# Kernel optimization log

Hardware: AMD Instinct MI355X
Metric: run time of the kernel (lower is better)

## Reference

```python
import jax, jax.numpy as jnp
import numpy as np

S, N, K = 8, 2048, 64          # snapshots, atoms, max neighbors (sum of max_num_neighs)
L = 20.0                        # periodic box length
R_CS, R_C = 6.0, 12.0           # smooth cutoff radii
M2 = 16                         # dim_sub_net


def _mlp(x, params, resnet=False):
    # DenseChainNet: Linear -> relu per layer; resnet skip when dims match or double (DeepMD style)
    for W, b in params:
        y = jax.nn.relu(x @ W + b)
        if resnet and y.shape[-1] == x.shape[-1]:
            y = y + x
        elif resnet and y.shape[-1] == 2 * x.shape[-1]:
            y = y + jnp.concatenate([x, x], axis=-1)
        x = y
    return x


def setup_inputs() -> dict:
    ks = jax.random.split(jax.random.key(0), 14)
    inputs = jax.random.uniform(ks[0], (S, N, 3), jnp.float32) * L
    input_types = jax.random.randint(ks[1], (S, N), 0, 2)
    nl = jax.random.randint(ks[2], (S, N, K), 0, N)
    neigh_list = jnp.where(jax.random.uniform(ks[3], (S, N, K)) < 0.2, -1, nl)  # -1 = padded neighbor

    def w(k, i, o):
        return jax.random.normal(k, (i, o), jnp.float32) / np.float32(np.sqrt(i))

    return {
        'inputs': inputs,
        'input_types': input_types,
        'neigh_list': neigh_list,
        'length': jnp.array([L, L, L], jnp.float32),
        # embed_species (species_dim [2,16,32])
        'ew0': w(ks[4], 2, 16), 'eb0': jnp.zeros((16,), jnp.float32),
        'ew1': w(ks[5], 16, 32), 'eb1': jnp.zeros((32,), jnp.float32),
        # fit_species (species_fit [32,32,31])
        'fw0': w(ks[6], 32, 32), 'fb0': jnp.zeros((32,), jnp.float32),
        'fw1': w(ks[7], 32, 31), 'fb1': jnp.zeros((31,), jnp.float32),
        # embed_net (descript_dim [32,64,128], resnet=True)
        'gw0': w(ks[8], 32, 64), 'gb0': jnp.zeros((64,), jnp.float32),
        'gw1': w(ks[9], 64, 128), 'gb1': jnp.zeros((128,), jnp.float32),
    }


def reference(inputs, input_types, neigh_list, length,
              ew0, eb0, ew1, eb1, fw0, fb0, fw1, fb1, gw0, gb0, gw1, gb1):
    mask = neigh_list == -1                                   # [S,N,K]
    idx = jnp.where(mask, 0, neigh_list)

    # ---- gen_coordinates_smooth: neighbor gather + min-image + smooth cutoff ----
    neigh_pos = jax.vmap(lambda p, i: p[i])(inputs, idx)      # [S,N,K,3]
    diff = neigh_pos - inputs[:, :, None, :]
    diff = diff - length * jnp.round(diff / length)           # minimum image convention
    rsq = jnp.sum(diff * diff, axis=-1)
    r = jnp.sqrt(jnp.where(rsq > 0, rsq, 1.0))                # safe sqrt (self/padded pairs)
    inv = 1.0 / r
    u = (r - R_CS) / (R_C - R_CS)
    sw = jnp.where(r < R_CS, inv,
                   jnp.where(r < R_C, inv * (0.5 * jnp.cos(jnp.pi * u) + 0.5), 0.0))
    valid = (~mask) & (rsq > 0)
    s_ij = jnp.where(valid, sw, 0.0)                          # [S,N,K]  s(r)
    r_ij = diff * (s_ij / r)[..., None]                       # [S,N,K,3] s(r)*x/r

    # ---- SpeciesModule: pair-type embedding (symmetrized) ----
    neigh_types = jax.vmap(lambda t, i: t[i])(input_types, idx)           # [S,N,K]
    center = jnp.broadcast_to(input_types[:, :, None], (S, N, K))
    pairs = jnp.stack([center, neigh_types], axis=-1).astype(jnp.float32).reshape(-1, 2)
    emb = [(ew0, eb0), (ew1, eb1)]
    t = _mlp(pairs, emb) + _mlp(pairs[:, ::-1], emb)
    td = _mlp(t, [(fw0, fb0), (fw1, fb1)]).reshape(S, N, K, -1)           # [S,N,K,31]
    td = jnp.where(mask[..., None], 0.0, td)

    # ---- embedding net + descriptor contraction ----
    s_tilde = jnp.concatenate([td, s_ij[..., None]], axis=-1)             # [S,N,K,32]
    G = _mlp(s_tilde.reshape(S * N * K, -1), [(gw0, gb0), (gw1, gb1)],
             resnet=True).reshape(S, N, K, -1)                            # [S,N,K,128]
    r_tilde = jnp.concatenate([s_ij[..., None], r_ij], axis=-1)           # [S,N,K,4]
    G2 = G[..., :M2]
    R = jnp.einsum('snkd,snkm->sndm', r_tilde, G2)                        # [S,N,4,16]
    R1 = jnp.einsum('snkd,sndm->snkm', r_tilde, R)                        # [S,N,K,16]
    D = jnp.einsum('snke,snkm->snem', G, R1)                              # [S,N,128,16]
    return D
```

## Files before the change

kernel.cpp:

```cpp
#include <hip/hip_runtime.h>
#include <math.h>

#define S_DIM 8
#define N_DIM 2048
#define K_DIM 64
#define APW 4
#define ST_ST 40
#define ST_H1 72

typedef __attribute__((ext_vector_type(8))) short bf16x8;
typedef __attribute__((ext_vector_type(4))) float f32x4;
typedef __attribute__((ext_vector_type(4))) int   i32x4;

__device__ __forceinline__ unsigned asu(float x) {
    union { float f; unsigned u; } v; v.f = x; return v.u;
}
__device__ __forceinline__ unsigned short f2bf(float x) {
    unsigned u = asu(x);
    return (unsigned short)((u + 0x7FFFu + ((u >> 16) & 1u)) >> 16);
}
__device__ __forceinline__ float bf2f(unsigned short h) {
    union { unsigned u; float f; } v; v.u = ((unsigned)h) << 16; return v.f;
}
__device__ __forceinline__ unsigned rne_pk(float x, float y) {
    unsigned ux = asu(x), uy = asu(y);
    return ((ux + 0x7FFFu + ((ux >> 16) & 1u)) >> 16) |
           ((uy + 0x7FFFu + ((uy >> 16) & 1u)) & 0xFFFF0000u);
}
__device__ __forceinline__ unsigned trn_pk(float x, float y) {
    return (asu(x) >> 16) | (asu(y) & 0xFFFF0000u);
}
__device__ __forceinline__ bf16x8 half_frag(unsigned p0, unsigned p1) {
    union { i32x4 i; bf16x8 b; } u;
    u.i = (i32x4){(int)p0, (int)p1, 0, 0};
    return u.b;
}

__global__ __launch_bounds__(256) void prep_kernel(
        const float* __restrict__ ew0, const float* __restrict__ eb0,
        const float* __restrict__ ew1, const float* __restrict__ eb1,
        const float* __restrict__ fw0, const float* __restrict__ fb0,
        const float* __restrict__ fw1, const float* __restrict__ fb1,
        const float* __restrict__ gw0, const float* __restrict__ gw1,
        unsigned* __restrict__ td_pk,
        unsigned short* __restrict__ w0t, unsigned short* __restrict__ w1t) {
    __shared__ float l_ew0[32], l_eb0[16], l_ew1[512], l_eb1[32];
    __shared__ float l_fw0[1024], l_fb0[32], l_fw1[992], l_fb1[31];
    __shared__ float l_h[4][2][16];
    __shared__ float l_tv[4][32];
    __shared__ float l_f1[4][32];
    __shared__ float l_td[4][32];

    const int tid = threadIdx.x;
    if (tid < 32) l_ew0[tid] = ew0[tid];
    if (tid < 16) l_eb0[tid] = eb0[tid];
    for (int i = tid; i < 512; i += 256) l_ew1[i] = ew1[i];
    if (tid < 32) l_eb1[tid] = eb1[tid];
    for (int i = tid; i < 1024; i += 256) l_fw0[i] = fw0[i];
    if (tid < 32) l_fb0[tid] = fb0[tid];
    for (int i = tid; i < 992; i += 256) l_fw1[i] = fw1[i];
    if (tid < 31) l_fb1[tid] = fb1[tid];
    __syncthreads();

    if (tid < 128) {
        const int p = tid >> 5, ord = (tid >> 4) & 1, j = tid & 15;
        const float c = (float)(p >> 1), t = (float)(p & 1);
        const float x0 = ord ? t : c;
        const float x1 = ord ? c : t;
        l_h[p][ord][j] = fmaxf(x0 * l_ew0[j] + x1 * l_ew0[16 + j] + l_eb0[j], 0.f);
    }
    __syncthreads();
    if (tid < 128) {
        const int p = tid >> 5, j = tid & 31;
        float acc = 0.f;
#pragma unroll
        for (int ord = 0; ord < 2; ord++) {
            float v = l_eb1[j];
#pragma unroll
            for (int i = 0; i < 16; i++) v += l_h[p][ord][i] * l_ew1[i * 32 + j];
            acc += fmaxf(v, 0.f);
        }
        l_tv[p][j] = acc;
    }
    __syncthreads();
    if (tid < 128) {
        const int p = tid >> 5, j = tid & 31;
        float v = l_fb0[j];
#pragma unroll
        for (int i = 0; i < 32; i++) v += l_tv[p][i] * l_fw0[i * 32 + j];
        l_f1[p][j] = fmaxf(v, 0.f);
    }
    __syncthreads();
    if (tid < 128) {
        const int p = tid >> 5, j = tid & 31;
        if (j < 31) {
            float v = l_fb1[j];
#pragma unroll
            for (int i = 0; i < 32; i++) v += l_f1[p][i] * l_fw1[i * 31 + j];
            l_td[p][j] = fmaxf(v, 0.f);
        } else {
            l_td[p][31] = 0.f;
        }
    }
    __syncthreads();
    if (tid < 64) {
        const int p = tid >> 4, i = tid & 15;
        const unsigned lo = f2bf(l_td[p][2 * i]);
        const unsigned hi = (i == 15) ? 0u : (unsigned)f2bf(l_td[p][2 * i + 1]);
        td_pk[tid] = lo | (hi << 16);
    }

    for (int idx = tid; idx < 2048; idx += 256) {
        const int j = idx >> 5, i = idx & 31;
        w0t[idx] = f2bf(gw0[i * 64 + j]);
    }
    for (int idx = tid; idx < 8192; idx += 256) {
        const int e = idx >> 6, j = idx & 63;
        w1t[idx] = f2bf(gw1[j * 128 + e]);
    }
}

__global__ __launch_bounds__(64, 2) void descr_mfma(
    const float* __restrict__ inputs, const int* __restrict__ input_types,
    const int* __restrict__ neigh_list, const float* __restrict__ length,
    const float* __restrict__ gb0, const float* __restrict__ gb1,
    const unsigned* __restrict__ td_pk, const unsigned short* __restrict__ w0t,
    const unsigned short* __restrict__ w1t, float* __restrict__ out)
{
    __shared__ __align__(16) unsigned short s_st[64 * ST_ST];
    __shared__ __align__(16) unsigned short s_h1[64 * ST_H1];
    __shared__ __align__(16) float s_rtT[4 * 68];
    __shared__ unsigned s_tdpk[64];
    float* s_A = (float*)s_st;

    const int lane = threadIdx.x;
    const int l15 = lane & 15;
    const int q = lane >> 4;

    bf16x8 w0f[4];
#pragma unroll
    for (int nt = 0; nt < 4; nt++)
        w0f[nt] = *(const bf16x8*)&w0t[(nt * 16 + l15) * 32 + q * 8];
    bf16x8 w1f[8][2];
#pragma unroll
    for (int et = 0; et < 8; et++) {
        w1f[et][0] = *(const bf16x8*)&w1t[(et * 16 + l15) * 64 + q * 8];
        w1f[et][1] = *(const bf16x8*)&w1t[(et * 16 + l15) * 64 + 32 + q * 8];
    }
    float b0f[4], b1f[8];
#pragma unroll
    for (int jt = 0; jt < 4; jt++) b0f[jt] = gb0[jt * 16 + l15];
#pragma unroll
    for (int et = 0; et < 8; et++) b1f[et] = gb1[et * 16 + l15];
    s_tdpk[lane] = td_pk[lane];
    const float Lx = length[0], Ly = length[1], Lz = length[2];
    const float iLx = 1.f / Lx, iLy = 1.f / Ly, iLz = 1.f / Lz;

    const f32x4 zf = {0.f, 0.f, 0.f, 0.f};

    for (int aa = 0; aa < APW; aa++) {
        const int atom = blockIdx.x * APW + aa;
        const int sidx = atom >> 11;

        __syncthreads();

        {
            const int nb = neigh_list[atom * K_DIM + lane];
            const bool msk = nb < 0;
            const int idx = msk ? 0 : nb;
            const float cx = inputs[atom * 3 + 0];
            const float cy = inputs[atom * 3 + 1];
            const float cz = inputs[atom * 3 + 2];
            const int nbase = (sidx * N_DIM + idx) * 3;
            float dx = inputs[nbase + 0] - cx;
            float dy = inputs[nbase + 1] - cy;
            float dz = inputs[nbase + 2] - cz;
            dx -= Lx * rintf(dx * iLx);
            dy -= Ly * rintf(dy * iLy);
            dz -= Lz * rintf(dz * iLz);
            const float rsq = dx * dx + dy * dy + dz * dz;
            const float r = sqrtf(rsq > 0.f ? rsq : 1.f);
            const float inv = 1.f / r;
            float sw;
            if (r < 6.f) sw = inv;
            else if (r < 12.f) {
                const float u = (r - 6.f) * (1.f / 6.f);
                sw = inv * (0.5f * __cosf(3.14159265358979323846f * u) + 0.5f);
            } else sw = 0.f;
            const bool valid = (!msk) && (rsq > 0.f);
            const float sij = valid ? sw : 0.f;
            const float f = sij * inv;
            s_rtT[0 * 68 + lane] = sij;
            s_rtT[1 * 68 + lane] = dx * f;
            s_rtT[2 * 68 + lane] = dy * f;
            s_rtT[3 * 68 + lane] = dz * f;

            const int ct = input_types[atom];
            const int ntp = input_types[sidx * N_DIM + idx];
            const unsigned* tdr = &s_tdpk[(ct * 2 + ntp) * 16];
            const unsigned zmask = msk ? 0u : 0xFFFFFFFFu;
            unsigned* strow = (unsigned*)&s_st[lane * ST_ST];
#pragma unroll
            for (int i = 0; i < 15; i++) strow[i] = tdr[i] & zmask;
            strow[15] = (tdr[15] & zmask & 0xFFFFu) | (((unsigned)f2bf(sij)) << 16);
            strow[16] = 0; strow[17] = 0; strow[18] = 0; strow[19] = 0;
        }
        __syncthreads();

        bf16x8 rtf[4];
#pragma unroll
        for (int a = 0; a < 4; a++) {
            const f32x4 rv = *(const f32x4*)&s_rtT[(l15 & 3) * 68 + a * 16 + q * 4];
            rtf[a] = half_frag(rne_pk(rv[0], rv[1]), rne_pk(rv[2], rv[3]));
        }

        f32x4 Bj[4] = {zf, zf, zf, zf};
#pragma unroll
        for (int mt = 0; mt < 4; mt++) {
            const bf16x8 afr = *(const bf16x8*)&s_st[(mt * 16 + l15) * ST_ST + q * 8];
            f32x4 c1[4];
#pragma unroll
            for (int jt = 0; jt < 4; jt++)
                c1[jt] = __builtin_amdgcn_mfma_f32_16x16x32_bf16(afr, w0f[jt], zf, 0, 0, 0);
#pragma unroll
            for (int jt = 0; jt < 4; jt++) {
                float hv[4];
#pragma unroll
                for (int reg = 0; reg < 4; reg++) {
                    const int k = mt * 16 + q * 4 + reg;
                    const float r = bf2f(s_st[k * ST_ST + (jt & 1) * 16 + l15]);
                    hv[reg] = fmaxf(c1[jt][reg] + b0f[jt], 0.f) + r;
                    s_h1[k * ST_H1 + jt * 16 + l15] = f2bf(hv[reg]);
                }
                const bf16x8 hf = half_frag(trn_pk(hv[0], hv[1]), trn_pk(hv[2], hv[3]));
                Bj[jt] = __builtin_amdgcn_mfma_f32_16x16x32_bf16(rtf[mt], hf, Bj[jt], 0, 0, 0);
            }
        }
        __syncthreads();

        f32x4 AT[8] = {zf, zf, zf, zf, zf, zf, zf, zf};
#pragma unroll
        for (int kt = 0; kt < 4; kt++) {
            const bf16x8 a0 = *(const bf16x8*)&s_h1[(kt * 16 + l15) * ST_H1 + q * 8];
            const bf16x8 a1 = *(const bf16x8*)&s_h1[(kt * 16 + l15) * ST_H1 + 32 + q * 8];
#pragma unroll
            for (int et = 0; et < 8; et++) {
                f32x4 c2 = __builtin_amdgcn_mfma_f32_16x16x32_bf16(a0, w1f[et][0], zf, 0, 0, 0);
                c2 = __builtin_amdgcn_mfma_f32_16x16x32_bf16(a1, w1f[et][1], c2, 0, 0, 0);
                const float g0 = fmaxf(c2[0] + b1f[et], 0.f);
                const float g1 = fmaxf(c2[1] + b1f[et], 0.f);
                const float g2 = fmaxf(c2[2] + b1f[et], 0.f);
                const float g3 = fmaxf(c2[3] + b1f[et], 0.f);
                const bf16x8 gf = half_frag(trn_pk(g0, g1), trn_pk(g2, g3));
                AT[et] = __builtin_amdgcn_mfma_f32_16x16x32_bf16(rtf[kt], gf, AT[et], 0, 0, 0);
            }
        }

        if (lane < 16) {
#pragma unroll
            for (int et = 0; et < 8; et++) {
                const f32x4 v = AT[et] + Bj[et & 3];
                *(f32x4*)&s_A[(et * 16 + lane) * 4] = v;
            }
        }
        __syncthreads();

        {
            const int m0 = (lane & 3) * 4;
            const int er = lane >> 2;
            f32x4 Am[4];
#pragma unroll
            for (int t = 0; t < 4; t++) Am[t] = *(const f32x4*)&s_A[(m0 + t) * 4];
            float* op = out + (size_t)atom * 2048;
#pragma unroll
            for (int g = 0; g < 8; g++) {
                const int e = g * 16 + er;
                const f32x4 Ae = *(const f32x4*)&s_A[e * 4];
                f32x4 o;
                o[0] = Ae[0]*Am[0][0] + Ae[1]*Am[0][1] + Ae[2]*Am[0][2] + Ae[3]*Am[0][3];
                o[1] = Ae[0]*Am[1][0] + Ae[1]*Am[1][1] + Ae[2]*Am[1][2] + Ae[3]*Am[1][3];
                o[2] = Ae[0]*Am[2][0] + Ae[1]*Am[2][1] + Ae[2]*Am[2][2] + Ae[3]*Am[2][3];
                o[3] = Ae[0]*Am[3][0] + Ae[1]*Am[3][1] + Ae[2]*Am[3][2] + Ae[3]*Am[3][3];
                *(f32x4*)&op[e * 16 + m0] = o;
            }
        }
    }
}

extern "C" void kernel_launch(void* const* d_in, const int* in_sizes, int n_in,
                              void* d_out, int out_size, void* d_ws, size_t ws_size,
                              hipStream_t stream) {
    (void)in_sizes; (void)n_in; (void)out_size; (void)ws_size;
    const float* inputs      = (const float*)d_in[0];
    const int*   input_types = (const int*)d_in[1];
    const int*   neigh_list  = (const int*)d_in[2];
    const float* length      = (const float*)d_in[3];
    const float* ew0 = (const float*)d_in[4];
    const float* eb0 = (const float*)d_in[5];
    const float* ew1 = (const float*)d_in[6];
    const float* eb1 = (const float*)d_in[7];
    const float* fw0 = (const float*)d_in[8];
    const float* fb0 = (const float*)d_in[9];
    const float* fw1 = (const float*)d_in[10];
    const float* fb1 = (const float*)d_in[11];
    const float* gw0 = (const float*)d_in[12];
    const float* gb0 = (const float*)d_in[13];
    const float* gw1 = (const float*)d_in[14];
    const float* gb1 = (const float*)d_in[15];
    float* out = (float*)d_out;

    unsigned* td_pk = (unsigned*)d_ws;
    unsigned short* w0t = (unsigned short*)((char*)d_ws + 512);
    unsigned short* w1t = (unsigned short*)((char*)d_ws + 512 + 4096);

    hipLaunchKernelGGL(prep_kernel, dim3(1), dim3(256), 0, stream,
                       ew0, eb0, ew1, eb1, fw0, fb0, fw1, fb1, gw0, gw1,
                       td_pk, w0t, w1t);

    const int nblocks = (S_DIM * N_DIM) / APW;
    hipLaunchKernelGGL(descr_mfma, dim3(nblocks), dim3(64), 0, stream,
                       inputs, input_types, neigh_list, length,
                       gb0, gb1, td_pk, w0t, w1t, out);
}
```

Measured before the change: 226.6 us.

## Prefetch next atom's inputs, interleave layer-2 per tile, replace barriers with LDS waits

The block is a single 64-lane wavefront, so the __syncthreads calls are replaced with an lgkmcnt wait plus a sched_barrier. The next atom's neighbor list, coordinates and types are software-prefetched into registers while the current atom computes. The second MLP layer now runs per 16-row tile right after the first, using a double-buffered 16-row h1 slab, which shrinks LDS. Launch bounds are raised to 3 waves per SIMD to allow more occupancy, at the risk of register pressure or spills.

```diff
diff --git a/kernel.cpp b/kernel.cpp
--- a/kernel.cpp
+++ b/kernel.cpp
@@ -30,10 +30,16 @@
 __device__ __forceinline__ unsigned trn_pk(float x, float y) {
     return (asu(x) >> 16) | (asu(y) & 0xFFFF0000u);
 }
-__device__ __forceinline__ bf16x8 half_frag(unsigned p0, unsigned p1) {
-    union { i32x4 i; bf16x8 b; } u;
-    u.i = (i32x4){(int)p0, (int)p1, 0, 0};
-    return u.b;
+__device__ __forceinline__ void lds_fence() {
+    asm volatile("s_waitcnt lgkmcnt(0)" ::: "memory");
+    __builtin_amdgcn_sched_barrier(0);
+}
+__device__ __forceinline__ f32x4 mfma_k16(unsigned a0, unsigned a1,
+                                          unsigned b0, unsigned b1, f32x4 c) {
+    union { i32x4 i; bf16x8 b; } ua, ub;
+    ua.i = (i32x4){(int)a0, (int)a1, 0, 0};
+    ub.i = (i32x4){(int)b0, (int)b1, 0, 0};
+    return __builtin_amdgcn_mfma_f32_16x16x32_bf16(ua.b, ub.b, c, 0, 0, 0);
 }
 
 __global__ __launch_bounds__(256) void prep_kernel(
@@ -120,7 +126,7 @@
     }
 }
 
-__global__ __launch_bounds__(64, 2) void descr_mfma(
+__global__ __launch_bounds__(64, 3) void descr_mfma(
     const float* __restrict__ inputs, const int* __restrict__ input_types,
     const int* __restrict__ neigh_list, const float* __restrict__ length,
     const float* __restrict__ gb0, const float* __restrict__ gb1,
@@ -128,7 +134,7 @@
     const unsigned short* __restrict__ w1t, float* __restrict__ out)
 {
     __shared__ __align__(16) unsigned short s_st[64 * ST_ST];
-    __shared__ __align__(16) unsigned short s_h1[64 * ST_H1];
+    __shared__ __align__(16) unsigned short s_h1[2][16 * ST_H1];
     __shared__ __align__(16) float s_rtT[4 * 68];
     __shared__ unsigned s_tdpk[64];
     float* s_A = (float*)s_st;
@@ -136,6 +142,8 @@
     const int lane = threadIdx.x;
     const int l15 = lane & 15;
     const int q = lane >> 4;
+    const int abase = blockIdx.x * APW;
+    const int sidx = abase >> 11;
 
     bf16x8 w0f[4];
 #pragma unroll
@@ -155,26 +163,39 @@
     s_tdpk[lane] = td_pk[lane];
     const float Lx = length[0], Ly = length[1], Lz = length[2];
     const float iLx = 1.f / Lx, iLy = 1.f / Ly, iLz = 1.f / Lz;
-
     const f32x4 zf = {0.f, 0.f, 0.f, 0.f};
 
+    int   cnb  = neigh_list[abase * K_DIM + lane];
+    float ccx  = inputs[abase * 3 + 0];
+    float ccy  = inputs[abase * 3 + 1];
+    float ccz  = inputs[abase * 3 + 2];
+    int   cct  = input_types[abase];
+    int   cidx0 = cnb < 0 ? 0 : cnb;
+    float cpx  = inputs[(sidx * N_DIM + cidx0) * 3 + 0];
+    float cpy  = inputs[(sidx * N_DIM + cidx0) * 3 + 1];
+    float cpz  = inputs[(sidx * N_DIM + cidx0) * 3 + 2];
+    int   cntp = input_types[sidx * N_DIM + cidx0];
+
     for (int aa = 0; aa < APW; aa++) {
-        const int atom = blockIdx.x * APW + aa;
-        const int sidx = atom >> 11;
-
-        __syncthreads();
+        const int atom = abase + aa;
+        const bool pf = (aa + 1 < APW);
+
+        int nnb = 0, nct = 0; float ncx = 0.f, ncy = 0.f, ncz = 0.f;
+        if (pf) {
+            nnb = neigh_list[(atom + 1) * K_DIM + lane];
+            ncx = inputs[(atom + 1) * 3 + 0];
+            ncy = inputs[(atom + 1) * 3 + 1];
+            ncz = inputs[(atom + 1) * 3 + 2];
+            nct = input_types[atom + 1];
+        }
+
+        lds_fence();
 
         {
-            const int nb = neigh_list[atom * K_DIM + lane];
-            const bool msk = nb < 0;
-            const int idx = msk ? 0 : nb;
-            const float cx = inputs[atom * 3 + 0];
-            const float cy = inputs[atom * 3 + 1];
-            const float cz = inputs[atom * 3 + 2];
-            const int nbase = (sidx * N_DIM + idx) * 3;
-            float dx = inputs[nbase + 0] - cx;
-            float dy = inputs[nbase + 1] - cy;
-            float dz = inputs[nbase + 2] - cz;
+            const bool msk = cnb < 0;
+            float dx = cpx - ccx;
+            float dy = cpy - ccy;
+            float dz = cpz - ccz;
             dx -= Lx * rintf(dx * iLx);
             dy -= Ly * rintf(dy * iLy);
             dz -= Lz * rintf(dz * iLz);
@@ -195,9 +216,7 @@
             s_rtT[2 * 68 + lane] = dy * f;
             s_rtT[3 * 68 + lane] = dz * f;
 
-            const int ct = input_types[atom];
-            const int ntp = input_types[sidx * N_DIM + idx];
-            const unsigned* tdr = &s_tdpk[(ct * 2 + ntp) * 16];
+            const unsigned* tdr = &s_tdpk[(cct * 2 + cntp) * 16];
             const unsigned zmask = msk ? 0u : 0xFFFFFFFFu;
             unsigned* strow = (unsigned*)&s_st[lane * ST_ST];
 #pragma unroll
@@ -205,18 +224,23 @@
             strow[15] = (tdr[15] & zmask & 0xFFFFu) | (((unsigned)f2bf(sij)) << 16);
             strow[16] = 0; strow[17] = 0; strow[18] = 0; strow[19] = 0;
         }
-        __syncthreads();
-
-        bf16x8 rtf[4];
+        lds_fence();
+
+        unsigned rtp[4][2];
 #pragma unroll
         for (int a = 0; a < 4; a++) {
             const f32x4 rv = *(const f32x4*)&s_rtT[(l15 & 3) * 68 + a * 16 + q * 4];
-            rtf[a] = half_frag(rne_pk(rv[0], rv[1]), rne_pk(rv[2], rv[3]));
-        }
-
+            rtp[a][0] = rne_pk(rv[0], rv[1]);
+            rtp[a][1] = rne_pk(rv[2], rv[3]);
+        }
+
+        int nidx = 0, nntp = 0; float npx = 0.f, npy = 0.f, npz = 0.f;
         f32x4 Bj[4] = {zf, zf, zf, zf};
+        f32x4 AT[8] = {zf, zf, zf, zf, zf, zf, zf, zf};
+
 #pragma unroll
         for (int mt = 0; mt < 4; mt++) {
+            unsigned short* h1c = s_h1[mt & 1];
             const bf16x8 afr = *(const bf16x8*)&s_st[(mt * 16 + l15) * ST_ST + q * 8];
             f32x4 c1[4];
 #pragma unroll
@@ -228,21 +252,25 @@
 #pragma unroll
                 for (int reg = 0; reg < 4; reg++) {
                     const int k = mt * 16 + q * 4 + reg;
-                    const float r = bf2f(s_st[k * ST_ST + (jt & 1) * 16 + l15]);
-                    hv[reg] = fmaxf(c1[jt][reg] + b0f[jt], 0.f) + r;
-                    s_h1[k * ST_H1 + jt * 16 + l15] = f2bf(hv[reg]);
+                    const float rres = bf2f(s_st[k * ST_ST + (jt & 1) * 16 + l15]);
+                    hv[reg] = fmaxf(c1[jt][reg] + b0f[jt], 0.f) + rres;
+                    h1c[(q * 4 + reg) * ST_H1 + jt * 16 + l15] = f2bf(hv[reg]);
                 }
-                const bf16x8 hf = half_frag(trn_pk(hv[0], hv[1]), trn_pk(hv[2], hv[3]));
-                Bj[jt] = __builtin_amdgcn_mfma_f32_16x16x32_bf16(rtf[mt], hf, Bj[jt], 0, 0, 0);
-            }
-        }
-        __syncthreads();
-
-        f32x4 AT[8] = {zf, zf, zf, zf, zf, zf, zf, zf};
-#pragma unroll
-        for (int kt = 0; kt < 4; kt++) {
-            const bf16x8 a0 = *(const bf16x8*)&s_h1[(kt * 16 + l15) * ST_H1 + q * 8];
-            const bf16x8 a1 = *(const bf16x8*)&s_h1[(kt * 16 + l15) * ST_H1 + 32 + q * 8];
+                Bj[jt] = mfma_k16(rtp[mt][0], rtp[mt][1],
+                                  trn_pk(hv[0], hv[1]), trn_pk(hv[2], hv[3]), Bj[jt]);
+            }
+            if (mt == 0 && pf) {
+                nidx = nnb < 0 ? 0 : nnb;
+                const int nbase = (sidx * N_DIM + nidx) * 3;
+                npx = inputs[nbase + 0];
+                npy = inputs[nbase + 1];
+                npz = inputs[nbase + 2];
+                nntp = input_types[sidx * N_DIM + nidx];
+            }
+            lds_fence();
+
+            const bf16x8 a0 = *(const bf16x8*)&h1c[l15 * ST_H1 + q * 8];
+            const bf16x8 a1 = *(const bf16x8*)&h1c[l15 * ST_H1 + 32 + q * 8];
 #pragma unroll
             for (int et = 0; et < 8; et++) {
                 f32x4 c2 = __builtin_amdgcn_mfma_f32_16x16x32_bf16(a0, w1f[et][0], zf, 0, 0, 0);
@@ -251,8 +279,8 @@
                 const float g1 = fmaxf(c2[1] + b1f[et], 0.f);
                 const float g2 = fmaxf(c2[2] + b1f[et], 0.f);
                 const float g3 = fmaxf(c2[3] + b1f[et], 0.f);
-                const bf16x8 gf = half_frag(trn_pk(g0, g1), trn_pk(g2, g3));
-                AT[et] = __builtin_amdgcn_mfma_f32_16x16x32_bf16(rtf[kt], gf, AT[et], 0, 0, 0);
+                AT[et] = mfma_k16(rtp[mt][0], rtp[mt][1],
+                                  trn_pk(g0, g1), trn_pk(g2, g3), AT[et]);
             }
         }
 
@@ -263,7 +291,7 @@
                 *(f32x4*)&s_A[(et * 16 + lane) * 4] = v;
             }
         }
-        __syncthreads();
+        lds_fence();
 
         {
             const int m0 = (lane & 3) * 4;
@@ -284,6 +312,9 @@
                 *(f32x4*)&op[e * 16 + m0] = o;
             }
         }
+
+        cnb = nnb; ccx = ncx; ccy = ncy; ccz = ncz; cct = nct;
+        cpx = npx; cpy = npy; cpz = npz; cntp = nntp;
     }
 }
 
```

Measured after the change: 373.9 us. +65.0%, slower.
